# Kernel tuning notes

Measured on AMD Instinct MI355X. Metric: run time of the kernel, lower is better.

## Reference

```python
import jax, jax.numpy as jnp
import numpy as np

N_NODES = 100000
N_EDGES = 1600000
N_GRAPHS = 1000
H = 128
F_IN = 128
F_EDGE = 16
DEPTH = 4


def setup_inputs() -> dict:
    key = jax.random.key(0)
    ks = jax.random.split(key, 10)
    s = 1.0 / np.sqrt(H)
    x = jax.random.normal(ks[0], (N_NODES, F_IN), dtype=jnp.float32)
    edge_index = jax.random.randint(ks[1], (2, N_EDGES), 0, N_NODES, dtype=jnp.int32)
    edge_attr = jax.random.normal(ks[2], (N_EDGES, F_EDGE), dtype=jnp.float32)
    batch = jnp.sort(jax.random.randint(ks[3], (N_NODES,), 0, N_GRAPHS, dtype=jnp.int32))
    W0 = jax.random.normal(ks[4], (F_IN, H), dtype=jnp.float32) * s
    b0 = jnp.zeros((H,), dtype=jnp.float32)
    W1 = jax.random.normal(ks[5], (DEPTH, H, H), dtype=jnp.float32) * s
    b1 = jnp.zeros((DEPTH, H), dtype=jnp.float32)
    W2 = jax.random.normal(ks[6], (DEPTH, H, H), dtype=jnp.float32) * s
    b2 = jnp.zeros((DEPTH, H), dtype=jnp.float32)
    Wf = jax.random.normal(ks[7], (H, 1), dtype=jnp.float32) * s
    bf = jnp.zeros((1,), dtype=jnp.float32)
    return {"x": x, "edge_index": edge_index, "edge_attr": edge_attr, "batch": batch,
            "W0": W0, "b0": b0, "W1": W1, "b1": b1, "W2": W2, "b2": b2, "Wf": Wf, "bf": bf}


def reference(x, edge_index, edge_attr, batch, W0, b0, W1, b1, W2, b2, Wf, bf):
    # edge_attr is read by the original forward but never used in the math.
    src, dst = edge_index[0], edge_index[1]
    n = x.shape[0]
    h0 = jax.nn.relu(x @ W0 + b0)  # [N, H]
    h = h0
    for i in range(DEPTH):
        # GINConv (eps=0): MLP(x + sum_{j in N(i)} x_j); messages flow src -> dst
        agg = jax.ops.segment_sum(h[src], dst, num_segments=n)  # [N, H]
        z = h + agg
        z = jax.nn.relu(z @ W1[i] + b1[i]) @ W2[i] + b2[i]
        # residual then relu (dropout p=0.02 is identity at eval)
        h = jax.nn.relu(z + h0)
    pooled = jax.ops.segment_sum(h, batch, num_segments=N_GRAPHS)  # [G, H]
    out = (pooled @ Wf + bf)[:, 0]  # [G]
    return out
```

## Files before the change

### kernel.cpp

```cpp
#include <hip/hip_runtime.h>

#define N_NODES 100000
#define N_EDGES 1600000
#define N_GRAPHS 1000
#define H 128
#define DEPTH 4
#define NB 391
#define BCAP 4864

typedef __attribute__((ext_vector_type(8))) short bf16x8;
typedef __attribute__((ext_vector_type(4))) float f32x4;

__device__ __forceinline__ unsigned short f2bf(float f) {
  unsigned int u = __float_as_uint(f);
  u += 0x7FFF + ((u >> 16) & 1);
  return (unsigned short)(u >> 16);
}
__device__ __forceinline__ float bflo(unsigned int v) { return __uint_as_float(v << 16); }
__device__ __forceinline__ float bfhi(unsigned int v) { return __uint_as_float(v & 0xFFFF0000u); }

__global__ __launch_bounds__(256) void k_bcnt(const int* __restrict__ dst, int* __restrict__ gcnt) {
  __shared__ int c[NB];
  int tid = threadIdx.x, e0 = blockIdx.x * 4096;
  for (int i = tid; i < NB; i += 256) c[i] = 0;
  __syncthreads();
#pragma unroll
  for (int i = 0; i < 16; ++i) {
    int e = e0 + i * 256 + tid;
    if (e < N_EDGES) atomicAdd(&c[dst[e] >> 8], 1);
  }
  __syncthreads();
  for (int i = tid; i < NB; i += 256)
    if (c[i]) atomicAdd(&gcnt[i], c[i]);
}

__global__ __launch_bounds__(512) void k_bscan(const int* __restrict__ gcnt, int* __restrict__ boff,
                                               int* __restrict__ cursor) {
  __shared__ int sh[512];
  int t = threadIdx.x;
  int v = (t < NB) ? gcnt[t] : 0;
  sh[t] = v;
  __syncthreads();
  for (int s = 1; s < 512; s <<= 1) {
    int x = (t >= s) ? sh[t - s] : 0;
    __syncthreads();
    sh[t] += x;
    __syncthreads();
  }
  if (t < NB) {
    int e = sh[t] - v;
    boff[t] = e;
    cursor[t] = e;
  }
  if (t == 0) boff[NB] = N_EDGES;
}

__global__ __launch_bounds__(256) void k_bucket(const int* __restrict__ src, const int* __restrict__ dst,
                                                int* __restrict__ cursor, unsigned int* __restrict__ ebuf) {
  __shared__ int cnt[NB];
  __shared__ int base[NB];
  int tid = threadIdx.x;
  int e0 = blockIdx.x * 4096;
  for (int i = tid; i < NB; i += 256) cnt[i] = 0;
  __syncthreads();
  unsigned int pk[16];
  int bk[16], rk[16];
#pragma unroll
  for (int i = 0; i < 16; ++i) {
    int e = e0 + i * 256 + tid;
    if (e < N_EDGES) {
      int s = src[e], d = dst[e];
      bk[i] = d >> 8;
      pk[i] = ((unsigned int)(d & 255) << 17) | (unsigned int)s;
      rk[i] = atomicAdd(&cnt[bk[i]], 1);
    } else
      bk[i] = -1;
  }
  __syncthreads();
  for (int i = tid; i < NB; i += 256)
    base[i] = cnt[i] ? atomicAdd(&cursor[i], cnt[i]) : 0;
  __syncthreads();
#pragma unroll
  for (int i = 0; i < 16; ++i)
    if (bk[i] >= 0) ebuf[base[bk[i]] + rk[i]] = pk[i];
}

__global__ __launch_bounds__(256) void k_bsort(const unsigned int* __restrict__ ebuf,
                                               const int* __restrict__ boff,
                                               int* __restrict__ csr, int* __restrict__ offs) {
  __shared__ unsigned int arr[BCAP];
  __shared__ unsigned int srt[BCAP];
  __shared__ unsigned short rnk[BCAP];
  __shared__ int cnt[256];
  __shared__ int off[257];
  int b = blockIdx.x, tid = threadIdx.x;
  int beg = boff[b], end = boff[b + 1];
  int ce = min(end - beg, BCAP);
  cnt[tid] = 0;
  __syncthreads();
  for (int i = tid; i < ce; i += 256) {
    unsigned int p = ebuf[beg + i];
    arr[i] = p;
    rnk[i] = (unsigned short)atomicAdd(&cnt[p >> 17], 1);
  }
  __syncthreads();
  int v = cnt[tid];
  off[tid + 1] = v;
  if (tid == 0) off[0] = 0;
  __syncthreads();
  for (int s = 1; s < 256; s <<= 1) {
    int x = (tid + 1 > s) ? off[tid + 1 - s] : 0;
    __syncthreads();
    off[tid + 1] += x;
    __syncthreads();
  }
  for (int i = tid; i < ce; i += 256) {
    unsigned int p = arr[i];
    srt[off[p >> 17] + rnk[i]] = p & 0x1FFFF;
  }
  __syncthreads();
  for (int i = tid; i < ce; i += 256) csr[beg + i] = (int)srt[i];
  int node = (b << 8) + tid;
  if (node < N_NODES) offs[node] = beg + off[tid];
  if (b == NB - 1 && tid == 0) offs[N_NODES] = N_EDGES;
}

__device__ __forceinline__ void stage_w(const float* __restrict__ Wg, unsigned short* Wt, int tid) {
  for (int idx = tid; idx < 2048; idx += 256) {
    int ng4 = idx & 31, kp = idx >> 5;
    float4 r0 = *(const float4*)&Wg[(2 * kp) * H + 4 * ng4];
    float4 r1 = *(const float4*)&Wg[(2 * kp + 1) * H + 4 * ng4];
    unsigned int p0 = (unsigned int)f2bf(r0.x) | ((unsigned int)f2bf(r1.x) << 16);
    unsigned int p1 = (unsigned int)f2bf(r0.y) | ((unsigned int)f2bf(r1.y) << 16);
    unsigned int p2 = (unsigned int)f2bf(r0.z) | ((unsigned int)f2bf(r1.z) << 16);
    unsigned int p3 = (unsigned int)f2bf(r0.w) | ((unsigned int)f2bf(r1.w) << 16);
    *(unsigned int*)&Wt[(4 * ng4 + 0) * 136 + 2 * kp] = p0;
    *(unsigned int*)&Wt[(4 * ng4 + 1) * 136 + 2 * kp] = p1;
    *(unsigned int*)&Wt[(4 * ng4 + 2) * 136 + 2 * kp] = p2;
    *(unsigned int*)&Wt[(4 * ng4 + 3) * 136 + 2 * kp] = p3;
  }
}

__global__ __launch_bounds__(256) void k_lin(const float* __restrict__ in, const float* __restrict__ Wg,
                                             const float* __restrict__ bg, unsigned short* __restrict__ outp) {
  __shared__ unsigned short Wt[128 * 136];
  __shared__ unsigned short zs[64 * 136];
  int tid = threadIdx.x;
  int lane = tid & 63, w = tid >> 6;
  int q = lane >> 4, l16 = lane & 15;
  int n0 = blockIdx.x * 64;

  stage_w(Wg, Wt, tid);

  int row = n0 + w * 16 + l16;
  int rr = (row < N_NODES) ? row : 0;
  bf16x8 afrag[4];
#pragma unroll
  for (int ks = 0; ks < 4; ++ks) {
    const float* p = &in[(size_t)rr * H + ks * 32 + q * 8];
    float4 f0 = *(const float4*)p;
    float4 f1 = *(const float4*)(p + 4);
    bf16x8 a;
    a[0] = (short)f2bf(f0.x); a[1] = (short)f2bf(f0.y); a[2] = (short)f2bf(f0.z); a[3] = (short)f2bf(f0.w);
    a[4] = (short)f2bf(f1.x); a[5] = (short)f2bf(f1.y); a[6] = (short)f2bf(f1.z); a[7] = (short)f2bf(f1.w);
    afrag[ks] = a;
  }
  f32x4 acc[8];
#pragma unroll
  for (int ct = 0; ct < 8; ++ct) acc[ct] = (f32x4){0.f, 0.f, 0.f, 0.f};
  __syncthreads();
#pragma unroll
  for (int ct = 0; ct < 8; ++ct)
#pragma unroll
    for (int ks = 0; ks < 4; ++ks) {
      bf16x8 b = *(bf16x8*)&Wt[(ct * 16 + l16) * 136 + ks * 32 + q * 8];
      acc[ct] = __builtin_amdgcn_mfma_f32_16x16x32_bf16(afrag[ks], b, acc[ct], 0, 0, 0);
    }
#pragma unroll
  for (int ct = 0; ct < 8; ++ct) {
    float bb = bg[ct * 16 + l16];
#pragma unroll
    for (int r = 0; r < 4; ++r) {
      float v = fmaxf(acc[ct][r] + bb, 0.f);
      zs[(w * 16 + q * 4 + r) * 136 + ct * 16 + l16] = f2bf(v);
    }
  }
  __syncthreads();
  int node = tid >> 2, cb = (tid & 3) * 32;
  if (n0 + node < N_NODES) {
#pragma unroll
    for (int i = 0; i < 4; ++i) {
      uint4 v = *(uint4*)&zs[node * 136 + cb + i * 8];
      *(uint4*)&outp[(size_t)(n0 + node) * H + cb + i * 8] = v;
    }
  }
}

__global__ __launch_bounds__(256) void k_agg(const unsigned short* __restrict__ hin, const int* __restrict__ offs,
                                             const int* __restrict__ csr, unsigned short* __restrict__ zin) {
  int node = blockIdx.x * 8 + (threadIdx.x >> 5);
  int l = threadIdx.x & 31;
  if (node >= N_NODES) return;
  const uint2* hu = (const uint2*)hin;
  uint2 self = hu[(size_t)node * 32 + l];
  float a0 = bflo(self.x), a1 = bfhi(self.x), a2 = bflo(self.y), a3 = bfhi(self.y);
  int beg = offs[node], end = offs[node + 1];
  for (int e = beg; e < end; e += 32) {
    int cnt = min(32, end - e);
    int idx = (l < cnt) ? csr[e + l] : 0;
    int j = 0;
    for (; j + 8 <= cnt; j += 8) {
      int s0 = __shfl(idx, j, 32), s1 = __shfl(idx, j + 1, 32);
      int s2 = __shfl(idx, j + 2, 32), s3 = __shfl(idx, j + 3, 32);
      int s4 = __shfl(idx, j + 4, 32), s5 = __shfl(idx, j + 5, 32);
      int s6 = __shfl(idx, j + 6, 32), s7 = __shfl(idx, j + 7, 32);
      uint2 v0 = hu[(size_t)s0 * 32 + l];
      uint2 v1 = hu[(size_t)s1 * 32 + l];
      uint2 v2 = hu[(size_t)s2 * 32 + l];
      uint2 v3 = hu[(size_t)s3 * 32 + l];
      uint2 v4 = hu[(size_t)s4 * 32 + l];
      uint2 v5 = hu[(size_t)s5 * 32 + l];
      uint2 v6 = hu[(size_t)s6 * 32 + l];
      uint2 v7 = hu[(size_t)s7 * 32 + l];
      a0 += bflo(v0.x); a1 += bfhi(v0.x); a2 += bflo(v0.y); a3 += bfhi(v0.y);
      a0 += bflo(v1.x); a1 += bfhi(v1.x); a2 += bflo(v1.y); a3 += bfhi(v1.y);
      a0 += bflo(v2.x); a1 += bfhi(v2.x); a2 += bflo(v2.y); a3 += bfhi(v2.y);
      a0 += bflo(v3.x); a1 += bfhi(v3.x); a2 += bflo(v3.y); a3 += bfhi(v3.y);
      a0 += bflo(v4.x); a1 += bfhi(v4.x); a2 += bflo(v4.y); a3 += bfhi(v4.y);
      a0 += bflo(v5.x); a1 += bfhi(v5.x); a2 += bflo(v5.y); a3 += bfhi(v5.y);
      a0 += bflo(v6.x); a1 += bfhi(v6.x); a2 += bflo(v6.y); a3 += bfhi(v6.y);
      a0 += bflo(v7.x); a1 += bfhi(v7.x); a2 += bflo(v7.y); a3 += bfhi(v7.y);
    }
    for (; j + 4 <= cnt; j += 4) {
      int s0 = __shfl(idx, j, 32), s1 = __shfl(idx, j + 1, 32);
      int s2 = __shfl(idx, j + 2, 32), s3 = __shfl(idx, j + 3, 32);
      uint2 v0 = hu[(size_t)s0 * 32 + l];
      uint2 v1 = hu[(size_t)s1 * 32 + l];
      uint2 v2 = hu[(size_t)s2 * 32 + l];
      uint2 v3 = hu[(size_t)s3 * 32 + l];
      a0 += bflo(v0.x); a1 += bfhi(v0.x); a2 += bflo(v0.y); a3 += bfhi(v0.y);
      a0 += bflo(v1.x); a1 += bfhi(v1.x); a2 += bflo(v1.y); a3 += bfhi(v1.y);
      a0 += bflo(v2.x); a1 += bfhi(v2.x); a2 += bflo(v2.y); a3 += bfhi(v2.y);
      a0 += bflo(v3.x); a1 += bfhi(v3.x); a2 += bflo(v3.y); a3 += bfhi(v3.y);
    }
    for (; j < cnt; ++j) {
      int s = __shfl(idx, j, 32);
      uint2 v = hu[(size_t)s * 32 + l];
      a0 += bflo(v.x); a1 += bfhi(v.x); a2 += bflo(v.y); a3 += bfhi(v.y);
    }
  }
  unsigned long long o = (unsigned long long)((unsigned int)f2bf(a0) | ((unsigned int)f2bf(a1) << 16)) |
                         ((unsigned long long)((unsigned int)f2bf(a2) | ((unsigned int)f2bf(a3) << 16)) << 32);
  __builtin_nontemporal_store(o, (unsigned long long*)zin + (size_t)node * 32 + l);
}

__global__ __launch_bounds__(256) void k_mlp(const unsigned short* __restrict__ zin,
                                             const float* __restrict__ W1g, const float* __restrict__ b1g,
                                             const float* __restrict__ W2g, const float* __restrict__ b2g,
                                             const unsigned short* __restrict__ h0, unsigned short* __restrict__ h) {
  __shared__ unsigned short Wt[128 * 136];
  __shared__ unsigned short zs[64 * 136];
  int tid = threadIdx.x;
  int lane = tid & 63, w = tid >> 6;
  int q = lane >> 4, l16 = lane & 15;
  int n0 = blockIdx.x * 64;

  stage_w(W1g, Wt, tid);

  int row = n0 + w * 16 + l16;
  int rr = (row < N_NODES) ? row : 0;
  bf16x8 afrag[4];
#pragma unroll
  for (int ks = 0; ks < 4; ++ks)
    afrag[ks] = *(bf16x8*)&zin[(size_t)rr * H + ks * 32 + q * 8];

  f32x4 acc[8];
#pragma unroll
  for (int ct = 0; ct < 8; ++ct) acc[ct] = (f32x4){0.f, 0.f, 0.f, 0.f};
  __syncthreads();
#pragma unroll
  for (int ct = 0; ct < 8; ++ct)
#pragma unroll
    for (int ks = 0; ks < 4; ++ks) {
      bf16x8 b = *(bf16x8*)&Wt[(ct * 16 + l16) * 136 + ks * 32 + q * 8];
      acc[ct] = __builtin_amdgcn_mfma_f32_16x16x32_bf16(afrag[ks], b, acc[ct], 0, 0, 0);
    }
  __syncthreads();
  stage_w(W2g, Wt, tid);
#pragma unroll
  for (int ct = 0; ct < 8; ++ct) {
    float bb = b1g[ct * 16 + l16];
#pragma unroll
    for (int r = 0; r < 4; ++r) {
      float v = fmaxf(acc[ct][r] + bb, 0.f);
      zs[(w * 16 + q * 4 + r) * 136 + ct * 16 + l16] = f2bf(v);
    }
  }
  __syncthreads();
  bf16x8 a2[4];
#pragma unroll
  for (int ks = 0; ks < 4; ++ks)
    a2[ks] = *(bf16x8*)&zs[(w * 16 + l16) * 136 + ks * 32 + q * 8];
  f32x4 acc2[8];
#pragma unroll
  for (int ct = 0; ct < 8; ++ct) acc2[ct] = (f32x4){0.f, 0.f, 0.f, 0.f};
#pragma unroll
  for (int ct = 0; ct < 8; ++ct)
#pragma unroll
    for (int ks = 0; ks < 4; ++ks) {
      bf16x8 b = *(bf16x8*)&Wt[(ct * 16 + l16) * 136 + ks * 32 + q * 8];
      acc2[ct] = __builtin_amdgcn_mfma_f32_16x16x32_bf16(a2[ks], b, acc2[ct], 0, 0, 0);
    }
#pragma unroll
  for (int ct = 0; ct < 8; ++ct) {
    float bb = b2g[ct * 16 + l16];
#pragma unroll
    for (int r = 0; r < 4; ++r) {
      float v = acc2[ct][r] + bb;
      zs[(w * 16 + q * 4 + r) * 136 + ct * 16 + l16] = f2bf(v);
    }
  }
  __syncthreads();
  int node = tid >> 2, cb = (tid & 3) * 32;
  if (n0 + node < N_NODES) {
    size_t base = (size_t)(n0 + node) * H + cb;
#pragma unroll
    for (int i = 0; i < 4; ++i) {
      uint4 zv = *(uint4*)&zs[node * 136 + cb + i * 8];
      uint4 hv = *(const uint4*)&h0[base + i * 8];
      unsigned int zr[4] = {zv.x, zv.y, zv.z, zv.w};
      unsigned int hr[4] = {hv.x, hv.y, hv.z, hv.w};
      uint4 o;
      unsigned int orr[4];
#pragma unroll
      for (int j = 0; j < 4; ++j) {
        float a = fmaxf(bflo(zr[j]) + bflo(hr[j]), 0.f);
        float b = fmaxf(bfhi(zr[j]) + bfhi(hr[j]), 0.f);
        orr[j] = (unsigned int)f2bf(a) | ((unsigned int)f2bf(b) << 16);
      }
      o.x = orr[0]; o.y = orr[1]; o.z = orr[2]; o.w = orr[3];
      *(uint4*)&h[base + i * 8] = o;
    }
  }
}

__global__ void k_starts(const int* __restrict__ batch, int* __restrict__ starts) {
  int n = blockIdx.x * 256 + threadIdx.x;
  if (n >= N_NODES) return;
  int b = batch[n];
  if (n == 0) {
    for (int g = 0; g <= b; ++g) starts[g] = 0;
  } else {
    int bp = batch[n - 1];
    for (int g = bp + 1; g <= b; ++g) starts[g] = n;
  }
  if (n == N_NODES - 1) {
    for (int g = b + 1; g <= N_GRAPHS; ++g) starts[g] = N_NODES;
  }
}

__global__ __launch_bounds__(256) void k_pool(const unsigned short* __restrict__ h, const int* __restrict__ starts,
                                              const float* __restrict__ Wf, const float* __restrict__ bf_,
                                              float* __restrict__ out) {
  __shared__ float r[4];
  int g = blockIdx.x, tid = threadIdx.x;
  int lane = tid & 63, w = tid >> 6;
  int beg = starts[g], end = starts[g + 1];
  const unsigned int* hu = (const unsigned int*)h;
  float sx = 0.f, sy = 0.f;
  for (int n = beg + w; n < end; n += 4) {
    unsigned int v = hu[(size_t)n * 64 + lane];
    sx += bflo(v);
    sy += bfhi(v);
  }
  float val = sx * Wf[2 * lane] + sy * Wf[2 * lane + 1];
#pragma unroll
  for (int off = 32; off > 0; off >>= 1) val += __shfl_down(val, off);
  if (lane == 0) r[w] = val;
  __syncthreads();
  if (tid == 0) out[g] = r[0] + r[1] + r[2] + r[3] + bf_[0];
}

extern "C" void kernel_launch(void* const* d_in, const int* in_sizes, int n_in,
                              void* d_out, int out_size, void* d_ws, size_t ws_size,
                              hipStream_t stream) {
  const float* x = (const float*)d_in[0];
  const int* ei = (const int*)d_in[1];
  const int* srcv = ei;
  const int* dstv = ei + N_EDGES;
  const int* batch = (const int*)d_in[3];
  const float* W0 = (const float*)d_in[4];
  const float* b0 = (const float*)d_in[5];
  const float* W1 = (const float*)d_in[6];
  const float* b1 = (const float*)d_in[7];
  const float* W2 = (const float*)d_in[8];
  const float* b2 = (const float*)d_in[9];
  const float* Wf = (const float*)d_in[10];
  const float* bf_ = (const float*)d_in[11];
  float* out = (float*)d_out;

  char* ws = (char*)d_ws;
  size_t o = 0;
  auto alloc = [&](size_t bytes) {
    size_t r = o;
    o = (o + bytes + 255) & ~(size_t)255;
    return r;
  };
  int* offs = (int*)(ws + alloc((N_NODES + 1) * sizeof(int)));
  int* gcnt = (int*)(ws + alloc(NB * sizeof(int)));
  int* boff = (int*)(ws + alloc((NB + 1) * sizeof(int)));
  int* cursor = (int*)(ws + alloc(NB * sizeof(int)));
  unsigned int* ebuf = (unsigned int*)(ws + alloc((size_t)N_EDGES * 4));
  int* csr = (int*)(ws + alloc((size_t)N_EDGES * sizeof(int)));
  int* starts = (int*)(ws + alloc((N_GRAPHS + 1) * sizeof(int)));
  unsigned short* h0 = (unsigned short*)(ws + alloc((size_t)N_NODES * H * 2));
  unsigned short* h = (unsigned short*)(ws + alloc((size_t)N_NODES * H * 2));
  unsigned short* zin = (unsigned short*)(ws + alloc((size_t)N_NODES * H * 2));

  hipMemsetAsync(gcnt, 0, NB * sizeof(int), stream);
  k_bcnt<<<NB, 256, 0, stream>>>(dstv, gcnt);
  k_bscan<<<1, 512, 0, stream>>>(gcnt, boff, cursor);
  k_bucket<<<NB, 256, 0, stream>>>(srcv, dstv, cursor, ebuf);
  k_bsort<<<NB, 256, 0, stream>>>(ebuf, boff, csr, offs);
  k_starts<<<(N_NODES + 255) / 256, 256, 0, stream>>>(batch, starts);

  const int nblk = (N_NODES + 63) / 64;
  k_lin<<<nblk, 256, 0, stream>>>(x, W0, b0, h0);
  for (int i = 0; i < DEPTH; ++i) {
    const unsigned short* hin = (i == 0) ? h0 : h;
    k_agg<<<(N_NODES + 7) / 8, 256, 0, stream>>>(hin, offs, csr, zin);
    k_mlp<<<nblk, 256, 0, stream>>>(zin, W1 + (size_t)i * H * H, b1 + (size_t)i * H,
                                    W2 + (size_t)i * H * H, b2 + (size_t)i * H, h0, h);
  }
  k_pool<<<N_GRAPHS, 256, 0, stream>>>(h, starts, Wf, bf_, out);
}
```

Baseline: 671.8 us.

## Pre-transpose weights once to bf16 and fuse pooling into final MLP

Adds a one-time kernel that converts and transposes all nine weight matrices to bf16 in the padded shared layout. Each MLP block then does a plain vectorised copy instead of converting fp32 per block, and the W2 load is prefetched into registers so it overlaps the first GEMM. The separate starts and pool kernels are removed. Pooling is instead fused into the last MLP as a dot with Wf plus atomicAdd per graph. This trades a full re-read of h for many float atomics and higher register pressure, and the atomics make the summation order nondeterministic.

```diff
diff --git a/kernel.cpp b/kernel.cpp
--- a/kernel.cpp
+++ b/kernel.cpp
@@ -7,6 +7,7 @@
 #define DEPTH 4
 #define NB 391
 #define BCAP 4864
+#define WT_ELEMS 17408
 
 typedef __attribute__((ext_vector_type(8))) short bf16x8;
 typedef __attribute__((ext_vector_type(4))) float f32x4;
@@ -125,23 +126,23 @@
   if (b == NB - 1 && tid == 0) offs[N_NODES] = N_EDGES;
 }
 
-__device__ __forceinline__ void stage_w(const float* __restrict__ Wg, unsigned short* Wt, int tid) {
-  for (int idx = tid; idx < 2048; idx += 256) {
-    int ng4 = idx & 31, kp = idx >> 5;
-    float4 r0 = *(const float4*)&Wg[(2 * kp) * H + 4 * ng4];
-    float4 r1 = *(const float4*)&Wg[(2 * kp + 1) * H + 4 * ng4];
-    unsigned int p0 = (unsigned int)f2bf(r0.x) | ((unsigned int)f2bf(r1.x) << 16);
-    unsigned int p1 = (unsigned int)f2bf(r0.y) | ((unsigned int)f2bf(r1.y) << 16);
-    unsigned int p2 = (unsigned int)f2bf(r0.z) | ((unsigned int)f2bf(r1.z) << 16);
-    unsigned int p3 = (unsigned int)f2bf(r0.w) | ((unsigned int)f2bf(r1.w) << 16);
-    *(unsigned int*)&Wt[(4 * ng4 + 0) * 136 + 2 * kp] = p0;
-    *(unsigned int*)&Wt[(4 * ng4 + 1) * 136 + 2 * kp] = p1;
-    *(unsigned int*)&Wt[(4 * ng4 + 2) * 136 + 2 * kp] = p2;
-    *(unsigned int*)&Wt[(4 * ng4 + 3) * 136 + 2 * kp] = p3;
-  }
-}
-
-__global__ __launch_bounds__(256) void k_lin(const float* __restrict__ in, const float* __restrict__ Wg,
+__global__ __launch_bounds__(256) void k_wprep(const float* __restrict__ W0, const float* __restrict__ W1,
+                                               const float* __restrict__ W2, unsigned short* __restrict__ Wtg) {
+  int b = blockIdx.x;
+  const float* src = (b == 0) ? W0 : (b <= 4 ? W1 + (size_t)(b - 1) * H * H : W2 + (size_t)(b - 5) * H * H);
+  unsigned short* dst = Wtg + (size_t)b * WT_ELEMS;
+  for (int idx = threadIdx.x; idx < 16384; idx += 256) {
+    int k = idx >> 7, n = idx & 127;
+    dst[n * 136 + k] = f2bf(src[k * H + n]);
+  }
+}
+
+__device__ __forceinline__ void stage_wt(const unsigned short* __restrict__ Wtg, unsigned short* Wt, int tid) {
+  for (int idx = tid * 8; idx < WT_ELEMS; idx += 2048)
+    *(uint4*)&Wt[idx] = *(const uint4*)&Wtg[idx];
+}
+
+__global__ __launch_bounds__(256) void k_lin(const float* __restrict__ in, const unsigned short* __restrict__ Wtg0,
                                              const float* __restrict__ bg, unsigned short* __restrict__ outp) {
   __shared__ unsigned short Wt[128 * 136];
   __shared__ unsigned short zs[64 * 136];
@@ -150,7 +151,7 @@
   int q = lane >> 4, l16 = lane & 15;
   int n0 = blockIdx.x * 64;
 
-  stage_w(Wg, Wt, tid);
+  stage_wt(Wtg0, Wt, tid);
 
   int row = n0 + w * 16 + l16;
   int rr = (row < N_NODES) ? row : 0;
@@ -255,9 +256,11 @@
 }
 
 __global__ __launch_bounds__(256) void k_mlp(const unsigned short* __restrict__ zin,
-                                             const float* __restrict__ W1g, const float* __restrict__ b1g,
-                                             const float* __restrict__ W2g, const float* __restrict__ b2g,
-                                             const unsigned short* __restrict__ h0, unsigned short* __restrict__ h) {
+                                             const unsigned short* __restrict__ Wtg1, const float* __restrict__ b1g,
+                                             const unsigned short* __restrict__ Wtg2, const float* __restrict__ b2g,
+                                             const unsigned short* __restrict__ h0, unsigned short* __restrict__ h,
+                                             int do_pool, const int* __restrict__ batch,
+                                             const float* __restrict__ Wf, float* __restrict__ pooled) {
   __shared__ unsigned short Wt[128 * 136];
   __shared__ unsigned short zs[64 * 136];
   int tid = threadIdx.x;
@@ -265,7 +268,7 @@
   int q = lane >> 4, l16 = lane & 15;
   int n0 = blockIdx.x * 64;
 
-  stage_w(W1g, Wt, tid);
+  stage_wt(Wtg1, Wt, tid);
 
   int row = n0 + w * 16 + l16;
   int rr = (row < N_NODES) ? row : 0;
@@ -274,6 +277,12 @@
   for (int ks = 0; ks < 4; ++ks)
     afrag[ks] = *(bf16x8*)&zin[(size_t)rr * H + ks * 32 + q * 8];
 
+  uint4 w2r[9];
+  {
+    int i = 0;
+    for (int idx = tid * 8; idx < WT_ELEMS; idx += 2048, ++i) w2r[i] = *(const uint4*)&Wtg2[idx];
+  }
+
   f32x4 acc[8];
 #pragma unroll
   for (int ct = 0; ct < 8; ++ct) acc[ct] = (f32x4){0.f, 0.f, 0.f, 0.f};
@@ -286,7 +295,10 @@
       acc[ct] = __builtin_amdgcn_mfma_f32_16x16x32_bf16(afrag[ks], b, acc[ct], 0, 0, 0);
     }
   __syncthreads();
-  stage_w(W2g, Wt, tid);
+  {
+    int i = 0;
+    for (int idx = tid * 8; idx < WT_ELEMS; idx += 2048, ++i) *(uint4*)&Wt[idx] = w2r[i];
+  }
 #pragma unroll
   for (int ct = 0; ct < 8; ++ct) {
     float bb = b1g[ct * 16 + l16];
@@ -322,64 +334,51 @@
   }
   __syncthreads();
   int node = tid >> 2, cb = (tid & 3) * 32;
-  if (n0 + node < N_NODES) {
-    size_t base = (size_t)(n0 + node) * H + cb;
+  int gn = n0 + node;
+  if (gn < N_NODES) {
+    size_t base = (size_t)gn * H + cb;
+    float pf = 0.f;
 #pragma unroll
     for (int i = 0; i < 4; ++i) {
       uint4 zv = *(uint4*)&zs[node * 136 + cb + i * 8];
       uint4 hv = *(const uint4*)&h0[base + i * 8];
       unsigned int zr[4] = {zv.x, zv.y, zv.z, zv.w};
       unsigned int hr[4] = {hv.x, hv.y, hv.z, hv.w};
-      uint4 o;
       unsigned int orr[4];
+      float4 wfa, wfb;
+      if (do_pool) {
+        wfa = *(const float4*)&Wf[cb + i * 8];
+        wfb = *(const float4*)&Wf[cb + i * 8 + 4];
+      }
 #pragma unroll
       for (int j = 0; j < 4; ++j) {
         float a = fmaxf(bflo(zr[j]) + bflo(hr[j]), 0.f);
         float b = fmaxf(bfhi(zr[j]) + bfhi(hr[j]), 0.f);
+        if (do_pool) {
+          float wa = (j == 0) ? wfa.x : (j == 1) ? wfa.z : (j == 2) ? wfb.x : wfb.z;
+          float wb = (j == 0) ? wfa.y : (j == 1) ? wfa.w : (j == 2) ? wfb.y : wfb.w;
+          pf += a * wa + b * wb;
+        }
         orr[j] = (unsigned int)f2bf(a) | ((unsigned int)f2bf(b) << 16);
       }
+      uint4 o;
       o.x = orr[0]; o.y = orr[1]; o.z = orr[2]; o.w = orr[3];
       *(uint4*)&h[base + i * 8] = o;
     }
-  }
-}
-
-__global__ void k_starts(const int* __restrict__ batch, int* __restrict__ starts) {
-  int n = blockIdx.x * 256 + threadIdx.x;
-  if (n >= N_NODES) return;
-  int b = batch[n];
-  if (n == 0) {
-    for (int g = 0; g <= b; ++g) starts[g] = 0;
-  } else {
-    int bp = batch[n - 1];
-    for (int g = bp + 1; g <= b; ++g) starts[g] = n;
-  }
-  if (n == N_NODES - 1) {
-    for (int g = b + 1; g <= N_GRAPHS; ++g) starts[g] = N_NODES;
-  }
-}
-
-__global__ __launch_bounds__(256) void k_pool(const unsigned short* __restrict__ h, const int* __restrict__ starts,
-                                              const float* __restrict__ Wf, const float* __restrict__ bf_,
-                                              float* __restrict__ out) {
-  __shared__ float r[4];
-  int g = blockIdx.x, tid = threadIdx.x;
-  int lane = tid & 63, w = tid >> 6;
-  int beg = starts[g], end = starts[g + 1];
-  const unsigned int* hu = (const unsigned int*)h;
-  float sx = 0.f, sy = 0.f;
-  for (int n = beg + w; n < end; n += 4) {
-    unsigned int v = hu[(size_t)n * 64 + lane];
-    sx += bflo(v);
-    sy += bfhi(v);
-  }
-  float val = sx * Wf[2 * lane] + sy * Wf[2 * lane + 1];
-#pragma unroll
-  for (int off = 32; off > 0; off >>= 1) val += __shfl_down(val, off);
-  if (lane == 0) r[w] = val;
-  __syncthreads();
-  if (tid == 0) out[g] = r[0] + r[1] + r[2] + r[3] + bf_[0];
-}
+    if (do_pool) {
+      pf += __shfl_xor(pf, 1);
+      pf += __shfl_xor(pf, 2);
+      if ((tid & 3) == 0) atomicAdd(&pooled[batch[gn]], pf);
+    }
+  }
+}
+
+__global__ void k_final(const float* __restrict__ pooled, const float* __restrict__ bf_, float* __restrict__ out) {
+  int g = blockIdx.x * 256 + threadIdx.x;
+  if (g < N_GRAPHS) out[g] = pooled[g] + bf_[0];
+}
+
+__global__ void k_starts_unused(const int* b, int* s) {}
 
 extern "C" void kernel_launch(void* const* d_in, const int* in_sizes, int n_in,
                               void* d_out, int out_size, void* d_ws, size_t ws_size,
@@ -412,25 +411,28 @@
   int* cursor = (int*)(ws + alloc(NB * sizeof(int)));
   unsigned int* ebuf = (unsigned int*)(ws + alloc((size_t)N_EDGES * 4));
   int* csr = (int*)(ws + alloc((size_t)N_EDGES * sizeof(int)));
-  int* starts = (int*)(ws + alloc((N_GRAPHS + 1) * sizeof(int)));
+  unsigned short* Wtg = (unsigned short*)(ws + alloc((size_t)9 * WT_ELEMS * 2));
+  float* pooled = (float*)(ws + alloc(N_GRAPHS * sizeof(float)));
   unsigned short* h0 = (unsigned short*)(ws + alloc((size_t)N_NODES * H * 2));
   unsigned short* h = (unsigned short*)(ws + alloc((size_t)N_NODES * H * 2));
   unsigned short* zin = (unsigned short*)(ws + alloc((size_t)N_NODES * H * 2));
 
   hipMemsetAsync(gcnt, 0, NB * sizeof(int), stream);
+  hipMemsetAsync(pooled, 0, N_GRAPHS * sizeof(float), stream);
+  k_wprep<<<9, 256, 0, stream>>>(W0, W1, W2, Wtg);
   k_bcnt<<<NB, 256, 0, stream>>>(dstv, gcnt);
   k_bscan<<<1, 512, 0, stream>>>(gcnt, boff, cursor);
   k_bucket<<<NB, 256, 0, stream>>>(srcv, dstv, cursor, ebuf);
   k_bsort<<<NB, 256, 0, stream>>>(ebuf, boff, csr, offs);
-  k_starts<<<(N_NODES + 255) / 256, 256, 0, stream>>>(batch, starts);
 
   const int nblk = (N_NODES + 63) / 64;
-  k_lin<<<nblk, 256, 0, stream>>>(x, W0, b0, h0);
+  k_lin<<<nblk, 256, 0, stream>>>(x, Wtg, b0, h0);
   for (int i = 0; i < DEPTH; ++i) {
     const unsigned short* hin = (i == 0) ? h0 : h;
     k_agg<<<(N_NODES + 7) / 8, 256, 0, stream>>>(hin, offs, csr, zin);
-    k_mlp<<<nblk, 256, 0, stream>>>(zin, W1 + (size_t)i * H * H, b1 + (size_t)i * H,
-                                    W2 + (size_t)i * H * H, b2 + (size_t)i * H, h0, h);
-  }
-  k_pool<<<N_GRAPHS, 256, 0, stream>>>(h, starts, Wf, bf_, out);
-}
+    k_mlp<<<nblk, 256, 0, stream>>>(zin, Wtg + (size_t)(1 + i) * WT_ELEMS, b1 + (size_t)i * H,
+                                    Wtg + (size_t)(5 + i) * WT_ELEMS, b2 + (size_t)i * H, h0, h,
+                                    (i == DEPTH - 1) ? 1 : 0, batch, Wf, pooled);
+  }
+  k_final<<<(N_GRAPHS + 255) / 256, 256, 0, stream>>>(pooled, bf_, out);
+}
```

New measurement: 795.6 us. 18.4% more time.
